# Kernel tuning notes

Measured on AMD Instinct MI355X. Metric: run time of the kernel, lower is better.

The kernel has to match this reference:

```python
import jax, jax.numpy as jnp
import numpy as np

N_NODES = 50000
N_EDGES = 600000
N_GRAPHS = 512
HID = 128
N_CLASSES = 10
N_LAYERS = 4
BN_EPS = 1e-5


def setup_inputs() -> dict:
    key = jax.random.key(0)
    ks = jax.random.split(key, 12)
    s = 1.0 / np.sqrt(HID)
    x = jax.random.normal(ks[0], (N_NODES, HID), dtype=jnp.float32)
    edge_index = jax.random.randint(ks[1], (2, N_EDGES), 0, N_NODES, dtype=jnp.int64)
    batch = jnp.sort(jax.random.randint(ks[2], (N_NODES,), 0, N_GRAPHS, dtype=jnp.int64))
    return {
        "x": x,
        "edge_index": edge_index,
        "batch": batch,
        # stacked SAGEConv params: lin_l (neighbor, with bias) and lin_r (root, no bias)
        "Wl": jax.random.uniform(ks[3], (N_LAYERS, HID, HID), jnp.float32, -s, s),
        "bl": jax.random.uniform(ks[4], (N_LAYERS, HID), jnp.float32, -s, s),
        "Wr": jax.random.uniform(ks[5], (N_LAYERS, HID, HID), jnp.float32, -s, s),
        # BatchNorm affine params per layer
        "gamma": jnp.ones((N_LAYERS, HID), jnp.float32),
        "beta": jnp.zeros((N_LAYERS, HID), jnp.float32),
        # classifier: Linear(HID, HID//2) -> ReLU -> Linear(HID//2, C)
        "W1": jax.random.uniform(ks[6], (HID // 2, HID), jnp.float32, -s, s),
        "b1": jax.random.uniform(ks[7], (HID // 2,), jnp.float32, -s, s),
        "W2": jax.random.uniform(ks[8], (N_CLASSES, HID // 2), jnp.float32, -1.0 / np.sqrt(HID // 2), 1.0 / np.sqrt(HID // 2)),
        "b2": jax.random.uniform(ks[9], (N_CLASSES,), jnp.float32, -1.0 / np.sqrt(HID // 2), 1.0 / np.sqrt(HID // 2)),
    }


def reference(x, edge_index, batch, Wl, bl, Wr, gamma, beta, W1, b1, W2, b2):
    src, dst = edge_index[0], edge_index[1]
    n = x.shape[0]
    # in-degree for mean aggregation (clamped to avoid div by zero)
    deg = jax.ops.segment_sum(jnp.ones(src.shape[0], x.dtype), dst, num_segments=n)
    inv_deg = 1.0 / jnp.maximum(deg, 1.0)  # [N]
    for l in range(Wl.shape[0]):
        # SAGEConv: mean-aggregate neighbor features, then lin_l(agg) + lin_r(x)
        agg = jax.ops.segment_sum(x[src], dst, num_segments=n) * inv_deg[:, None]  # [N,H]
        h = agg @ Wl[l].T + bl[l] + x @ Wr[l].T  # [N,H]
        # BatchNorm1d (training-mode batch stats, biased variance)
        mu = h.mean(axis=0)
        var = h.var(axis=0)
        h = (h - mu) * jax.lax.rsqrt(var + BN_EPS) * gamma[l] + beta[l]
        x = jax.nn.relu(h)  # dropout is identity in eval/reference
    # global mean pool over graphs
    cnt = jax.ops.segment_sum(jnp.ones(n, x.dtype), batch, num_segments=N_GRAPHS)
    pooled = jax.ops.segment_sum(x, batch, num_segments=N_GRAPHS) / jnp.maximum(cnt, 1.0)[:, None]
    h = jax.nn.relu(pooled @ W1.T + b1)
    return h @ W2.T + b2  # [G, C]
```

## Files before the change

kernel.cpp:

```cpp
#include <hip/hip_runtime.h>

#define NNODES 50000
#define MPAD   50048
#define NEDGES 600000
#define NGRAPHS 512
#define HID 128
#define NLAYERS 4
#define BN_EPS 1e-5f
#define GEMMBLK 391
#define PROWS 25

typedef __bf16 bf16x8 __attribute__((ext_vector_type(8)));
typedef float  f32x4  __attribute__((ext_vector_type(4)));
typedef unsigned short u16x8 __attribute__((ext_vector_type(8)));

__device__ __forceinline__ unsigned short f2bf(float f) {
    unsigned u = __builtin_bit_cast(unsigned, f);
    unsigned r = (u + 0x7fffu + ((u >> 16) & 1u)) >> 16;
    return (unsigned short)r;
}
__device__ __forceinline__ float bf2f(unsigned short u) {
    return __builtin_bit_cast(float, (unsigned)u << 16);
}

__global__ void k_init(int* __restrict__ deg,
                       int* __restrict__ pa, int* __restrict__ pb,
                       int* __restrict__ pc, int* __restrict__ pd,
                       int* __restrict__ pooled, int* __restrict__ gcnt) {
    int t = blockIdx.x * 256 + threadIdx.x;
    if (t < 50000) { deg[t] = 0; }
    int u = t - 50000;
    if (u >= 0 && u < 3072) { pa[u] = 0; pb[u] = 0; pc[u] = 0; pd[u] = 0; }
    int v = t - 53072;
    if (v >= 0 && v < 65536) pooled[v] = 0;
    int w = t - 118608;
    if (w >= 0 && w < 512) gcnt[w] = 0;
}

__global__ void k_count_deg(const int* __restrict__ dst, int* __restrict__ deg, int E) {
    int e = blockIdx.x * blockDim.x + threadIdx.x;
    if (e < E) atomicAdd(&deg[dst[e]], 1);
}

__global__ void k_scan1(const int* __restrict__ deg, int* __restrict__ exg,
                        int* __restrict__ bsum, int n) {
    __shared__ int s[512];
    int tid = threadIdx.x;
    int i = blockIdx.x * 512 + tid;
    int v = (i < n) ? deg[i] : 0;
    s[tid] = v;
    __syncthreads();
    for (int off = 1; off < 512; off <<= 1) {
        int t = (tid >= off) ? s[tid - off] : 0;
        __syncthreads();
        s[tid] += t;
        __syncthreads();
    }
    if (i < n) exg[i] = s[tid] - v;
    if (tid == 511) bsum[blockIdx.x] = s[511];
}

__global__ void k_scan2(int* __restrict__ bsum, int nb) {
    __shared__ int s[128];
    int tid = threadIdx.x;
    int v = (tid < nb) ? bsum[tid] : 0;
    s[tid] = v;
    __syncthreads();
    for (int off = 1; off < 128; off <<= 1) {
        int t = (tid >= off) ? s[tid - off] : 0;
        __syncthreads();
        s[tid] += t;
        __syncthreads();
    }
    if (tid < nb) bsum[tid] = s[tid] - v;
}

__global__ void k_scan3(const int* __restrict__ exg, const int* __restrict__ bsum,
                        const int* __restrict__ deg,
                        int* __restrict__ rowptr, int* __restrict__ cursor,
                        float* __restrict__ inv_deg, int n, int E) {
    int i = blockIdx.x * blockDim.x + threadIdx.x;
    if (i < n) {
        int r = exg[i] + bsum[i >> 9];
        rowptr[i] = r;
        cursor[i] = r;
        int d = deg[i];
        inv_deg[i] = 1.0f / (float)max(d, 1);
        if (i == 0) rowptr[n] = E;
    }
}

__global__ void k_fill_csr(const int* __restrict__ src, const int* __restrict__ dst,
                           int* __restrict__ cursor, int* __restrict__ csr_src, int E) {
    int e = blockIdx.x * blockDim.x + threadIdx.x;
    if (e < E) {
        int pos = atomicAdd(&cursor[dst[e]], 1);
        csr_src[pos] = src[e];
    }
}

__global__ void k_split(const float* __restrict__ x,
                        unsigned short* __restrict__ xhi, unsigned short* __restrict__ xlo) {
    int idx = blockIdx.x * 256 + threadIdx.x;
    float4 v = ((const float4*)x)[idx];
    ushort4 h, l;
    h.x = f2bf(v.x); l.x = f2bf(v.x - bf2f(h.x));
    h.y = f2bf(v.y); l.y = f2bf(v.y - bf2f(h.y));
    h.z = f2bf(v.z); l.z = f2bf(v.z - bf2f(h.z));
    h.w = f2bf(v.w); l.w = f2bf(v.w - bf2f(h.w));
    *(ushort4*)(xhi + (size_t)idx * 4) = h;
    *(ushort4*)(xlo + (size_t)idx * 4) = l;
}

__global__ void k_wpack(const float* __restrict__ Wl, const float* __restrict__ Wr,
                        unsigned short* __restrict__ Wpk) {
    int lane = threadIdx.x;
    int b = blockIdx.x;
    int nf = b & 7, ks = (b >> 3) & 7, l = b >> 6;
    int n = nf * 16 + (lane & 15);
    int k = ks * 32 + (lane >> 4) * 8;
    const float* W = (k < 128) ? (Wl + (size_t)l * HID * HID)
                               : (Wr + (size_t)l * HID * HID - 128);
    size_t base = ((((size_t)l * 64 + ks * 8 + nf) * 2) * 64 + lane) * 8;
    #pragma unroll
    for (int j = 0; j < 8; ++j) {
        float w = W[(size_t)n * 128 + k + j];
        unsigned short h = f2bf(w);
        unsigned short lo = f2bf(w - bf2f(h));
        Wpk[base + j] = h;
        Wpk[base + 512 + j] = lo;
    }
}

__global__ void k_aggregate5(const unsigned short* __restrict__ xhi,
                             const int* __restrict__ csr_src, const int* __restrict__ rowptr,
                             const float* __restrict__ inv_deg,
                             unsigned short* __restrict__ ahi, unsigned short* __restrict__ alo) {
    int lane = threadIdx.x & 63;
    int wid = threadIdx.x >> 6;
    int node = blockIdx.x * 4 + wid;
    int beg = rowptr[node];
    int deg = rowptr[node + 1] - beg;
    int eg = lane >> 4;
    int fo = (lane & 15) * 8;

    int idx_l = (lane < deg) ? csr_src[beg + lane] : 0;

    float acc0[8] = {0.f, 0.f, 0.f, 0.f, 0.f, 0.f, 0.f, 0.f};
    float acc1[8] = {0.f, 0.f, 0.f, 0.f, 0.f, 0.f, 0.f, 0.f};
    int dmax = min(deg, 64);
    for (int base = 0; base < dmax; base += 8) {
        int s0 = __shfl(idx_l, base + eg);
        int s1 = __shfl(idx_l, base + 4 + eg);
        if (base + eg < deg) {
            u16x8 v = *(const u16x8*)(xhi + (size_t)s0 * 128 + fo);
            #pragma unroll
            for (int j = 0; j < 8; ++j) acc0[j] += bf2f(v[j]);
        }
        if (base + 4 + eg < deg) {
            u16x8 v = *(const u16x8*)(xhi + (size_t)s1 * 128 + fo);
            #pragma unroll
            for (int j = 0; j < 8; ++j) acc1[j] += bf2f(v[j]);
        }
    }
    for (int e = beg + 64 + eg; e < beg + deg; e += 4) {
        int s = csr_src[e];
        u16x8 v = *(const u16x8*)(xhi + (size_t)s * 128 + fo);
        #pragma unroll
        for (int j = 0; j < 8; ++j) acc0[j] += bf2f(v[j]);
    }

    #pragma unroll
    for (int j = 0; j < 8; ++j) {
        float a = acc0[j] + acc1[j];
        a += __shfl_xor(a, 16);
        a += __shfl_xor(a, 32);
        acc0[j] = a;
    }
    if (lane < 16) {
        float idg = inv_deg[node];
        u16x8 hv, lv;
        #pragma unroll
        for (int j = 0; j < 8; ++j) {
            float a = acc0[j] * idg;
            unsigned short h = f2bf(a);
            hv[j] = h;
            lv[j] = f2bf(a - bf2f(h));
        }
        *(u16x8*)(ahi + (size_t)node * 128 + fo) = hv;
        *(u16x8*)(alo + (size_t)node * 128 + fo) = lv;
    }
}

__launch_bounds__(256) __global__
void k_mfma_gemm(const unsigned short* __restrict__ Ahi0, const unsigned short* __restrict__ Alo0,
                 const unsigned short* __restrict__ Ahi1, const unsigned short* __restrict__ Alo1,
                 const unsigned short* __restrict__ Wpk, const float* __restrict__ bl,
                 float* __restrict__ Hout,
                 float* __restrict__ psum, float* __restrict__ pqsum) {
    int wid = threadIdx.x >> 6;
    int lane = threadIdx.x & 63;
    int m0 = blockIdx.x * 128 + wid * 32;
    int r = lane & 15;
    int kg = lane >> 4;

    f32x4 acc[2][8];
    #pragma unroll
    for (int nf = 0; nf < 8; ++nf) {
        float b = bl[nf * 16 + r];
        acc[0][nf] = f32x4{b, b, b, b};
        acc[1][nf] = f32x4{b, b, b, b};
    }

    #pragma unroll
    for (int ks = 0; ks < 8; ++ks) {
        const unsigned short* hi = (ks < 4) ? Ahi0 : Ahi1;
        const unsigned short* lo = (ks < 4) ? Alo0 : Alo1;
        int kc = (ks & 3) * 32 + kg * 8;
        bf16x8 ah0 = *(const bf16x8*)(hi + (size_t)(m0 + r) * 128 + kc);
        bf16x8 al0 = *(const bf16x8*)(lo + (size_t)(m0 + r) * 128 + kc);
        bf16x8 ah1 = *(const bf16x8*)(hi + (size_t)(m0 + 16 + r) * 128 + kc);
        bf16x8 al1 = *(const bf16x8*)(lo + (size_t)(m0 + 16 + r) * 128 + kc);
        const unsigned short* wb = Wpk + (size_t)ks * 8192;
        #pragma unroll
        for (int nf = 0; nf < 8; ++nf) {
            bf16x8 bh = *(const bf16x8*)(wb + (size_t)nf * 1024 + lane * 8);
            bf16x8 bl2 = *(const bf16x8*)(wb + (size_t)nf * 1024 + 512 + lane * 8);
            acc[0][nf] = __builtin_amdgcn_mfma_f32_16x16x32_bf16(ah0, bh,  acc[0][nf], 0, 0, 0);
            acc[0][nf] = __builtin_amdgcn_mfma_f32_16x16x32_bf16(al0, bh,  acc[0][nf], 0, 0, 0);
            acc[0][nf] = __builtin_amdgcn_mfma_f32_16x16x32_bf16(ah0, bl2, acc[0][nf], 0, 0, 0);
            acc[1][nf] = __builtin_amdgcn_mfma_f32_16x16x32_bf16(ah1, bh,  acc[1][nf], 0, 0, 0);
            acc[1][nf] = __builtin_amdgcn_mfma_f32_16x16x32_bf16(al1, bh,  acc[1][nf], 0, 0, 0);
            acc[1][nf] = __builtin_amdgcn_mfma_f32_16x16x32_bf16(ah1, bl2, acc[1][nf], 0, 0, 0);
        }
    }

    #pragma unroll
    for (int mf = 0; mf < 2; ++mf)
        #pragma unroll
        for (int nf = 0; nf < 8; ++nf)
            #pragma unroll
            for (int g = 0; g < 4; ++g)
                Hout[(size_t)(m0 + mf * 16 + kg * 4 + g) * 128 + nf * 16 + r] = acc[mf][nf][g];

    __shared__ float ls[4][8][16];
    __shared__ float lq[4][8][16];
    #pragma unroll
    for (int nf = 0; nf < 8; ++nf) {
        float ss = 0.f, qq = 0.f;
        #pragma unroll
        for (int mf = 0; mf < 2; ++mf)
            #pragma unroll
            for (int g = 0; g < 4; ++g) {
                int row = m0 + mf * 16 + kg * 4 + g;
                float v = acc[mf][nf][g];
                float msk = (row < NNODES) ? 1.f : 0.f;
                ss += v * msk;
                qq += v * v * msk;
            }
        ss += __shfl_xor(ss, 16);
        ss += __shfl_xor(ss, 32);
        qq += __shfl_xor(qq, 16);
        qq += __shfl_xor(qq, 32);
        if (lane < 16) { ls[wid][nf][lane] = ss; lq[wid][nf][lane] = qq; }
    }
    __syncthreads();
    int t = threadIdx.x;
    if (t < 128) {
        int nf = t >> 4, rr = t & 15;
        float ssum = ls[0][nf][rr] + ls[1][nf][rr] + ls[2][nf][rr] + ls[3][nf][rr];
        float qsum = lq[0][nf][rr] + lq[1][nf][rr] + lq[2][nf][rr] + lq[3][nf][rr];
        psum[(size_t)t * GEMMBLK + blockIdx.x] = ssum;
        pqsum[(size_t)t * GEMMBLK + blockIdx.x] = qsum;
    }
}

__global__ void k_bnfin2(const float* __restrict__ psum, const float* __restrict__ pqsum,
                         const float* __restrict__ gamma, const float* __restrict__ beta,
                         float* __restrict__ scale, float* __restrict__ shift) {
    int c = blockIdx.x;
    int t = threadIdx.x;
    float s = 0.f, q = 0.f;
    const float* ps = psum + (size_t)c * GEMMBLK;
    const float* pq = pqsum + (size_t)c * GEMMBLK;
    for (int b = t; b < GEMMBLK; b += 64) { s += ps[b]; q += pq[b]; }
    #pragma unroll
    for (int off = 32; off; off >>= 1) {
        s += __shfl_xor(s, off);
        q += __shfl_xor(q, off);
    }
    if (t == 0) {
        float inv_n = 1.0f / (float)NNODES;
        float mu = s * inv_n;
        float var = q * inv_n - mu * mu;
        float is = rsqrtf(var + BN_EPS);
        float g = gamma[c] * is;
        scale[c] = g;
        shift[c] = beta[c] - mu * g;
    }
}

__global__ void k_bnrelu2(const float* __restrict__ h, const float* __restrict__ scale,
                          const float* __restrict__ shift,
                          unsigned short* __restrict__ xhi, unsigned short* __restrict__ xlo) {
    int idx = blockIdx.x * 256 + threadIdx.x;
    int cv = idx & 31;
    float4 sc = ((const float4*)scale)[cv];
    float4 sh = ((const float4*)shift)[cv];
    float4 v = ((const float4*)h)[idx];
    v.x = fmaxf(v.x * sc.x + sh.x, 0.f);
    v.y = fmaxf(v.y * sc.y + sh.y, 0.f);
    v.z = fmaxf(v.z * sc.z + sh.z, 0.f);
    v.w = fmaxf(v.w * sc.w + sh.w, 0.f);
    ushort4 hh, ll;
    hh.x = f2bf(v.x); ll.x = f2bf(v.x - bf2f(hh.x));
    hh.y = f2bf(v.y); ll.y = f2bf(v.y - bf2f(hh.y));
    hh.z = f2bf(v.z); ll.z = f2bf(v.z - bf2f(hh.z));
    hh.w = f2bf(v.w); ll.w = f2bf(v.w - bf2f(hh.w));
    *(ushort4*)(xhi + (size_t)idx * 4) = hh;
    *(ushort4*)(xlo + (size_t)idx * 4) = ll;
}

__global__ void k_pool_seg(const unsigned short* __restrict__ xhi,
                           const unsigned short* __restrict__ xlo,
                           const int* __restrict__ batch,
                           float* __restrict__ pooled, int* __restrict__ gcnt) {
    int t = threadIdx.x;
    int r0 = blockIdx.x * PROWS;
    float a0 = 0.f, a1 = 0.f;
    int cur = batch[r0];
    int seg = r0;
    for (int i = 0; i < PROWS; ++i) {
        int r = r0 + i;
        int g = batch[r];
        if (g != cur) {
            atomicAdd(&pooled[cur * 128 + 2 * t], a0);
            atomicAdd(&pooled[cur * 128 + 2 * t + 1], a1);
            if (t == 0) atomicAdd(&gcnt[cur], r - seg);
            a0 = a1 = 0.f; cur = g; seg = r;
        }
        unsigned uh = *(const unsigned*)(xhi + (size_t)r * 128 + 2 * t);
        unsigned ul = *(const unsigned*)(xlo + (size_t)r * 128 + 2 * t);
        a0 += bf2f((unsigned short)(uh & 0xffff)) + bf2f((unsigned short)(ul & 0xffff));
        a1 += bf2f((unsigned short)(uh >> 16)) + bf2f((unsigned short)(ul >> 16));
    }
    atomicAdd(&pooled[cur * 128 + 2 * t], a0);
    atomicAdd(&pooled[cur * 128 + 2 * t + 1], a1);
    if (t == 0) atomicAdd(&gcnt[cur], r0 + PROWS - seg);
}

__global__ void k_cls(const float* __restrict__ pooled, const int* __restrict__ gcnt,
                      const float* __restrict__ W1, const float* __restrict__ b1,
                      const float* __restrict__ W2, const float* __restrict__ b2,
                      float* __restrict__ out) {
    int g = blockIdx.x;
    int t = threadIdx.x;
    __shared__ float P[128];
    __shared__ float H1[64];
    float inv = 1.0f / (float)max(gcnt[g], 1);
    P[t] = pooled[g * 128 + t] * inv;
    P[t + 64] = pooled[g * 128 + 64 + t] * inv;
    __syncthreads();
    float a = b1[t];
    #pragma unroll 8
    for (int k = 0; k < 128; ++k) a += P[k] * W1[t * 128 + k];
    H1[t] = fmaxf(a, 0.f);
    __syncthreads();
    if (t < 10) {
        float a2 = b2[t];
        #pragma unroll 8
        for (int k = 0; k < 64; ++k) a2 += H1[k] * W2[t * 64 + k];
        out[g * 10 + t] = a2;
    }
}

extern "C" void kernel_launch(void* const* d_in, const int* in_sizes, int n_in,
                              void* d_out, int out_size, void* d_ws, size_t ws_size,
                              hipStream_t stream) {
    const float* x_in  = (const float*)d_in[0];
    const int*   ei    = (const int*)d_in[1];
    const int*   batch = (const int*)d_in[2];
    const float* Wl    = (const float*)d_in[3];
    const float* bl    = (const float*)d_in[4];
    const float* Wr    = (const float*)d_in[5];
    const float* gamma = (const float*)d_in[6];
    const float* beta  = (const float*)d_in[7];
    const float* W1    = (const float*)d_in[8];
    const float* b1    = (const float*)d_in[9];
    const float* W2    = (const float*)d_in[10];
    const float* b2    = (const float*)d_in[11];
    float* out = (float*)d_out;

    const int N = NNODES, E = NEDGES;
    const int* src = ei;
    const int* dst = ei + E;

    char* p = (char*)d_ws;
    auto alloc = [&](size_t bytes) {
        char* r = p;
        p += (bytes + 255) & ~(size_t)255;
        return r;
    };
    unsigned short* ahi = (unsigned short*)alloc((size_t)MPAD * HID * 2);
    unsigned short* alo = (unsigned short*)alloc((size_t)MPAD * HID * 2);
    unsigned short* xhi = (unsigned short*)alloc((size_t)MPAD * HID * 2);
    unsigned short* xlo = (unsigned short*)alloc((size_t)MPAD * HID * 2);
    float*  h        = (float*)alloc((size_t)MPAD * HID * 4);
    unsigned short* wpk = (unsigned short*)alloc((size_t)NLAYERS * 64 * 2 * 64 * 8 * 2);
    int*    deg      = (int*)alloc((size_t)N * 4);
    float*  inv_deg  = (float*)alloc((size_t)N * 4);
    int*    rowptr   = (int*)alloc((size_t)(N + 1) * 4);
    int*    cursor   = (int*)alloc((size_t)N * 4);
    int*    csr_src  = (int*)alloc((size_t)E * 4);
    int*    exg      = (int*)alloc((size_t)N * 4);
    int*    bsum     = (int*)alloc(512);
    float*  psum     = (float*)alloc((size_t)HID * GEMMBLK * 4);
    float*  pqsum    = (float*)alloc((size_t)HID * GEMMBLK * 4);
    float*  scale    = (float*)alloc(HID * 4);
    float*  shift    = (float*)alloc(HID * 4);
    float*  pooled   = (float*)alloc((size_t)NGRAPHS * HID * 4);
    int*    gcnt     = (int*)alloc((size_t)NGRAPHS * 4);

    k_init<<<502, 256, 0, stream>>>(deg,
                                    (int*)(ahi + (size_t)N * HID), (int*)(alo + (size_t)N * HID),
                                    (int*)(xhi + (size_t)N * HID), (int*)(xlo + (size_t)N * HID),
                                    (int*)pooled, gcnt);

    int eb = (E + 255) / 256;
    k_count_deg<<<eb, 256, 0, stream>>>(dst, deg, E);
    int nb = (N + 511) / 512;
    k_scan1<<<nb, 512, 0, stream>>>(deg, exg, bsum, N);
    k_scan2<<<1, 128, 0, stream>>>(bsum, nb);
    k_scan3<<<(N + 255) / 256, 256, 0, stream>>>(exg, bsum, deg, rowptr, cursor, inv_deg, N, E);
    k_fill_csr<<<eb, 256, 0, stream>>>(src, dst, cursor, csr_src, E);

    k_wpack<<<NLAYERS * 64, 64, 0, stream>>>(Wl, Wr, wpk);
    k_split<<<(N * HID / 4) / 256, 256, 0, stream>>>(x_in, xhi, xlo);

    for (int l = 0; l < NLAYERS; ++l) {
        k_aggregate5<<<N / 4, 256, 0, stream>>>(xhi, csr_src, rowptr, inv_deg, ahi, alo);
        k_mfma_gemm<<<GEMMBLK, 256, 0, stream>>>(ahi, alo, xhi, xlo,
                                                 wpk + (size_t)l * 65536,
                                                 bl + (size_t)l * HID, h, psum, pqsum);
        k_bnfin2<<<HID, 64, 0, stream>>>(psum, pqsum, gamma + (size_t)l * HID,
                                         beta + (size_t)l * HID, scale, shift);
        k_bnrelu2<<<(N * HID / 4) / 256, 256, 0, stream>>>(h, scale, shift, xhi, xlo);
    }

    k_pool_seg<<<N / PROWS, 64, 0, stream>>>(xhi, xlo, batch, pooled, gcnt);
    k_cls<<<NGRAPHS, 64, 0, stream>>>(pooled, gcnt, W1, b1, W2, b2, out);
}
```

Measured before the change: 379.4 us.

## Fuse GEMM, BatchNorm statistics and BN-ReLU into one kernel with grid barrier

Merges the MFMA GEMM, the BatchNorm finalize and the BN+ReLU+bf16 split into a single per-layer kernel. The three steps are joined by a software grid-wide atomic barrier, so the fp32 `h` intermediate never goes to global memory. This removes a full write and read-back of the hidden activations and two kernel launches per layer. In exchange, every block redundantly reduces the per-block partial sums. The final bf16 stores are narrower 2-byte scattered writes, and correctness relies on all 391 blocks being co-resident for the spin barrier.

```diff
diff --git a/kernel.cpp b/kernel.cpp
--- a/kernel.cpp
+++ b/kernel.cpp
@@ -26,7 +26,8 @@
 __global__ void k_init(int* __restrict__ deg,
                        int* __restrict__ pa, int* __restrict__ pb,
                        int* __restrict__ pc, int* __restrict__ pd,
-                       int* __restrict__ pooled, int* __restrict__ gcnt) {
+                       int* __restrict__ pooled, int* __restrict__ gcnt,
+                       unsigned* __restrict__ bar) {
     int t = blockIdx.x * 256 + threadIdx.x;
     if (t < 50000) { deg[t] = 0; }
     int u = t - 50000;
@@ -35,6 +36,8 @@
     if (v >= 0 && v < 65536) pooled[v] = 0;
     int w = t - 118608;
     if (w >= 0 && w < 512) gcnt[w] = 0;
+    int b = t - 119120;
+    if (b >= 0 && b < NLAYERS) bar[b] = 0u;
 }
 
 __global__ void k_count_deg(const int* __restrict__ dst, int* __restrict__ deg, int E) {
@@ -192,12 +195,13 @@
     }
 }
 
-__launch_bounds__(256) __global__
-void k_mfma_gemm(const unsigned short* __restrict__ Ahi0, const unsigned short* __restrict__ Alo0,
-                 const unsigned short* __restrict__ Ahi1, const unsigned short* __restrict__ Alo1,
-                 const unsigned short* __restrict__ Wpk, const float* __restrict__ bl,
-                 float* __restrict__ Hout,
-                 float* __restrict__ psum, float* __restrict__ pqsum) {
+__launch_bounds__(256, 2) __global__
+void k_layer(const unsigned short* __restrict__ Ahi, const unsigned short* __restrict__ Alo,
+             unsigned short* __restrict__ Xhi, unsigned short* __restrict__ Xlo,
+             const unsigned short* __restrict__ Wpk, const float* __restrict__ bl,
+             const float* __restrict__ gamma, const float* __restrict__ beta,
+             float* __restrict__ psum, float* __restrict__ pqsum,
+             unsigned* __restrict__ bar) {
     int wid = threadIdx.x >> 6;
     int lane = threadIdx.x & 63;
     int m0 = blockIdx.x * 128 + wid * 32;
@@ -214,8 +218,8 @@
 
     #pragma unroll
     for (int ks = 0; ks < 8; ++ks) {
-        const unsigned short* hi = (ks < 4) ? Ahi0 : Ahi1;
-        const unsigned short* lo = (ks < 4) ? Alo0 : Alo1;
+        const unsigned short* hi = (ks < 4) ? Ahi : Xhi;
+        const unsigned short* lo = (ks < 4) ? Alo : Xlo;
         int kc = (ks & 3) * 32 + kg * 8;
         bf16x8 ah0 = *(const bf16x8*)(hi + (size_t)(m0 + r) * 128 + kc);
         bf16x8 al0 = *(const bf16x8*)(lo + (size_t)(m0 + r) * 128 + kc);
@@ -234,14 +238,6 @@
             acc[1][nf] = __builtin_amdgcn_mfma_f32_16x16x32_bf16(ah1, bl2, acc[1][nf], 0, 0, 0);
         }
     }
-
-    #pragma unroll
-    for (int mf = 0; mf < 2; ++mf)
-        #pragma unroll
-        for (int nf = 0; nf < 8; ++nf)
-            #pragma unroll
-            for (int g = 0; g < 4; ++g)
-                Hout[(size_t)(m0 + mf * 16 + kg * 4 + g) * 128 + nf * 16 + r] = acc[mf][nf][g];
 
     __shared__ float ls[4][8][16];
     __shared__ float lq[4][8][16];
@@ -270,55 +266,61 @@
         int nf = t >> 4, rr = t & 15;
         float ssum = ls[0][nf][rr] + ls[1][nf][rr] + ls[2][nf][rr] + ls[3][nf][rr];
         float qsum = lq[0][nf][rr] + lq[1][nf][rr] + lq[2][nf][rr] + lq[3][nf][rr];
-        psum[(size_t)t * GEMMBLK + blockIdx.x] = ssum;
-        pqsum[(size_t)t * GEMMBLK + blockIdx.x] = qsum;
-    }
-}
-
-__global__ void k_bnfin2(const float* __restrict__ psum, const float* __restrict__ pqsum,
-                         const float* __restrict__ gamma, const float* __restrict__ beta,
-                         float* __restrict__ scale, float* __restrict__ shift) {
-    int c = blockIdx.x;
-    int t = threadIdx.x;
-    float s = 0.f, q = 0.f;
-    const float* ps = psum + (size_t)c * GEMMBLK;
-    const float* pq = pqsum + (size_t)c * GEMMBLK;
-    for (int b = t; b < GEMMBLK; b += 64) { s += ps[b]; q += pq[b]; }
-    #pragma unroll
-    for (int off = 32; off; off >>= 1) {
-        s += __shfl_xor(s, off);
-        q += __shfl_xor(q, off);
-    }
+        psum[(size_t)blockIdx.x * 128 + t] = ssum;
+        pqsum[(size_t)blockIdx.x * 128 + t] = qsum;
+    }
+
+    __threadfence();
+    __syncthreads();
     if (t == 0) {
+        __hip_atomic_fetch_add(bar, 1u, __ATOMIC_ACQ_REL, __HIP_MEMORY_SCOPE_AGENT);
+        while (__hip_atomic_load(bar, __ATOMIC_ACQUIRE, __HIP_MEMORY_SCOPE_AGENT) < (unsigned)GEMMBLK)
+            __builtin_amdgcn_s_sleep(2);
+    }
+    __syncthreads();
+    __threadfence();
+
+    __shared__ float sS[256], sQ[256];
+    __shared__ float scaleS[128], shiftS[128];
+    {
+        float s = 0.f, q = 0.f;
+        int c = t & 127;
+        for (int b = (t >> 7); b < GEMMBLK; b += 2) {
+            s += psum[(size_t)b * 128 + c];
+            q += pqsum[(size_t)b * 128 + c];
+        }
+        sS[t] = s; sQ[t] = q;
+    }
+    __syncthreads();
+    if (t < 128) {
+        float ss = sS[t] + sS[t + 128];
+        float qq = sQ[t] + sQ[t + 128];
         float inv_n = 1.0f / (float)NNODES;
-        float mu = s * inv_n;
-        float var = q * inv_n - mu * mu;
+        float mu = ss * inv_n;
+        float var = qq * inv_n - mu * mu;
         float is = rsqrtf(var + BN_EPS);
-        float g = gamma[c] * is;
-        scale[c] = g;
-        shift[c] = beta[c] - mu * g;
-    }
-}
-
-__global__ void k_bnrelu2(const float* __restrict__ h, const float* __restrict__ scale,
-                          const float* __restrict__ shift,
-                          unsigned short* __restrict__ xhi, unsigned short* __restrict__ xlo) {
-    int idx = blockIdx.x * 256 + threadIdx.x;
-    int cv = idx & 31;
-    float4 sc = ((const float4*)scale)[cv];
-    float4 sh = ((const float4*)shift)[cv];
-    float4 v = ((const float4*)h)[idx];
-    v.x = fmaxf(v.x * sc.x + sh.x, 0.f);
-    v.y = fmaxf(v.y * sc.y + sh.y, 0.f);
-    v.z = fmaxf(v.z * sc.z + sh.z, 0.f);
-    v.w = fmaxf(v.w * sc.w + sh.w, 0.f);
-    ushort4 hh, ll;
-    hh.x = f2bf(v.x); ll.x = f2bf(v.x - bf2f(hh.x));
-    hh.y = f2bf(v.y); ll.y = f2bf(v.y - bf2f(hh.y));
-    hh.z = f2bf(v.z); ll.z = f2bf(v.z - bf2f(hh.z));
-    hh.w = f2bf(v.w); ll.w = f2bf(v.w - bf2f(hh.w));
-    *(ushort4*)(xhi + (size_t)idx * 4) = hh;
-    *(ushort4*)(xlo + (size_t)idx * 4) = ll;
+        float g = gamma[t] * is;
+        scaleS[t] = g;
+        shiftS[t] = beta[t] - mu * g;
+    }
+    __syncthreads();
+
+    #pragma unroll
+    for (int mf = 0; mf < 2; ++mf)
+        #pragma unroll
+        for (int nf = 0; nf < 8; ++nf) {
+            int col = nf * 16 + r;
+            float sc = scaleS[col];
+            float sh = shiftS[col];
+            #pragma unroll
+            for (int g = 0; g < 4; ++g) {
+                int row = m0 + mf * 16 + kg * 4 + g;
+                float v = fmaxf(acc[mf][nf][g] * sc + sh, 0.f);
+                unsigned short hh = f2bf(v);
+                Xhi[(size_t)row * 128 + col] = hh;
+                Xlo[(size_t)row * 128 + col] = f2bf(v - bf2f(hh));
+            }
+        }
 }
 
 __global__ void k_pool_seg(const unsigned short* __restrict__ xhi,
@@ -405,7 +407,6 @@
     unsigned short* alo = (unsigned short*)alloc((size_t)MPAD * HID * 2);
     unsigned short* xhi = (unsigned short*)alloc((size_t)MPAD * HID * 2);
     unsigned short* xlo = (unsigned short*)alloc((size_t)MPAD * HID * 2);
-    float*  h        = (float*)alloc((size_t)MPAD * HID * 4);
     unsigned short* wpk = (unsigned short*)alloc((size_t)NLAYERS * 64 * 2 * 64 * 8 * 2);
     int*    deg      = (int*)alloc((size_t)N * 4);
     float*  inv_deg  = (float*)alloc((size_t)N * 4);
@@ -416,15 +417,14 @@
     int*    bsum     = (int*)alloc(512);
     float*  psum     = (float*)alloc((size_t)HID * GEMMBLK * 4);
     float*  pqsum    = (float*)alloc((size_t)HID * GEMMBLK * 4);
-    float*  scale    = (float*)alloc(HID * 4);
-    float*  shift    = (float*)alloc(HID * 4);
     float*  pooled   = (float*)alloc((size_t)NGRAPHS * HID * 4);
     int*    gcnt     = (int*)alloc((size_t)NGRAPHS * 4);
+    unsigned* bar    = (unsigned*)alloc(NLAYERS * 4);
 
     k_init<<<502, 256, 0, stream>>>(deg,
                                     (int*)(ahi + (size_t)N * HID), (int*)(alo + (size_t)N * HID),
                                     (int*)(xhi + (size_t)N * HID), (int*)(xlo + (size_t)N * HID),
-                                    (int*)pooled, gcnt);
+                                    (int*)pooled, gcnt, bar);
 
     int eb = (E + 255) / 256;
     k_count_deg<<<eb, 256, 0, stream>>>(dst, deg, E);
@@ -439,12 +439,11 @@
 
     for (int l = 0; l < NLAYERS; ++l) {
         k_aggregate5<<<N / 4, 256, 0, stream>>>(xhi, csr_src, rowptr, inv_deg, ahi, alo);
-        k_mfma_gemm<<<GEMMBLK, 256, 0, stream>>>(ahi, alo, xhi, xlo,
-                                                 wpk + (size_t)l * 65536,
-                                                 bl + (size_t)l * HID, h, psum, pqsum);
-        k_bnfin2<<<HID, 64, 0, stream>>>(psum, pqsum, gamma + (size_t)l * HID,
-                                         beta + (size_t)l * HID, scale, shift);
-        k_bnrelu2<<<(N * HID / 4) / 256, 256, 0, stream>>>(h, scale, shift, xhi, xlo);
+        k_layer<<<GEMMBLK, 256, 0, stream>>>(ahi, alo, xhi, xlo,
+                                             wpk + (size_t)l * 65536,
+                                             bl + (size_t)l * HID,
+                                             gamma + (size_t)l * HID, beta + (size_t)l * HID,
+                                             psum, pqsum, bar + l);
     }
 
     k_pool_seg<<<N / PROWS, 64, 0, stream>>>(xhi, xlo, batch, pooled, gcnt);
```

Measured after the change: 882.4 us. 2.33x slower.

## Store node features in 32-column blocks and aggregate one feature block per pass

Applied to the files above, without the earlier changes.

Node feature and aggregate buffers (hi/lo bf16 splits) change from row-major 128-wide rows to four feature blocks of 32 columns each. The neighbor-mean aggregation then runs four passes, one per block, so each gather touches a smaller working set that has a better chance of staying in L2. The split, BN/ReLU, GEMM, pooling and padding-zeroing kernels are all rewritten to use the new indexing. The trade-off is 64-byte gathers instead of 256-byte ones, four times as many aggregation blocks, and CSR indices that are re-read on every pass.

```diff
diff --git a/kernel.cpp b/kernel.cpp
--- a/kernel.cpp
+++ b/kernel.cpp
@@ -9,6 +9,7 @@
 #define BN_EPS 1e-5f
 #define GEMMBLK 391
 #define PROWS 25
+#define FBLK  (MPAD * 32)
 
 typedef __bf16 bf16x8 __attribute__((ext_vector_type(8)));
 typedef float  f32x4  __attribute__((ext_vector_type(4)));
@@ -22,6 +23,7 @@
 __device__ __forceinline__ float bf2f(unsigned short u) {
     return __builtin_bit_cast(float, (unsigned)u << 16);
 }
+
 
 __global__ void k_init(int* __restrict__ deg,
                        int* __restrict__ pa, int* __restrict__ pb,
@@ -30,7 +32,11 @@
     int t = blockIdx.x * 256 + threadIdx.x;
     if (t < 50000) { deg[t] = 0; }
     int u = t - 50000;
-    if (u >= 0 && u < 3072) { pa[u] = 0; pb[u] = 0; pc[u] = 0; pd[u] = 0; }
+    if (u >= 0 && u < 3072) {
+        int blk = u / 768, off = u - blk * 768;
+        int idx = blk * (MPAD * 16) + 50000 * 16 + off;
+        pa[idx] = 0; pb[idx] = 0; pc[idx] = 0; pd[idx] = 0;
+    }
     int v = t - 53072;
     if (v >= 0 && v < 65536) pooled[v] = 0;
     int w = t - 118608;
@@ -102,14 +108,16 @@
 __global__ void k_split(const float* __restrict__ x,
                         unsigned short* __restrict__ xhi, unsigned short* __restrict__ xlo) {
     int idx = blockIdx.x * 256 + threadIdx.x;
+    int row = idx >> 5, q = idx & 31;
     float4 v = ((const float4*)x)[idx];
     ushort4 h, l;
     h.x = f2bf(v.x); l.x = f2bf(v.x - bf2f(h.x));
     h.y = f2bf(v.y); l.y = f2bf(v.y - bf2f(h.y));
     h.z = f2bf(v.z); l.z = f2bf(v.z - bf2f(h.z));
     h.w = f2bf(v.w); l.w = f2bf(v.w - bf2f(h.w));
-    *(ushort4*)(xhi + (size_t)idx * 4) = h;
-    *(ushort4*)(xlo + (size_t)idx * 4) = l;
+    size_t dst = (size_t)(q >> 3) * FBLK + (size_t)row * 32 + (q & 7) * 4;
+    *(ushort4*)(xhi + dst) = h;
+    *(ushort4*)(xlo + dst) = l;
 }
 
 __global__ void k_wpack(const float* __restrict__ Wl, const float* __restrict__ Wr,
@@ -132,69 +140,65 @@
     }
 }
 
-__global__ void k_aggregate5(const unsigned short* __restrict__ xhi,
+__global__ void k_aggregate6(const unsigned short* __restrict__ xhi,
                              const int* __restrict__ csr_src, const int* __restrict__ rowptr,
                              const float* __restrict__ inv_deg,
                              unsigned short* __restrict__ ahi, unsigned short* __restrict__ alo) {
     int lane = threadIdx.x & 63;
     int wid = threadIdx.x >> 6;
-    int node = blockIdx.x * 4 + wid;
+    int nb   = blockIdx.x % 12500;
+    int pass = blockIdx.x / 12500;
+    int node = nb * 4 + wid;
     int beg = rowptr[node];
     int deg = rowptr[node + 1] - beg;
-    int eg = lane >> 4;
-    int fo = (lane & 15) * 8;
+    int slot = lane >> 2;
+    int f    = lane & 3;
+    size_t bb = (size_t)pass * FBLK;
 
     int idx_l = (lane < deg) ? csr_src[beg + lane] : 0;
 
-    float acc0[8] = {0.f, 0.f, 0.f, 0.f, 0.f, 0.f, 0.f, 0.f};
-    float acc1[8] = {0.f, 0.f, 0.f, 0.f, 0.f, 0.f, 0.f, 0.f};
+    float acc[8] = {0.f, 0.f, 0.f, 0.f, 0.f, 0.f, 0.f, 0.f};
     int dmax = min(deg, 64);
-    for (int base = 0; base < dmax; base += 8) {
-        int s0 = __shfl(idx_l, base + eg);
-        int s1 = __shfl(idx_l, base + 4 + eg);
-        if (base + eg < deg) {
-            u16x8 v = *(const u16x8*)(xhi + (size_t)s0 * 128 + fo);
+    for (int base = 0; base < dmax; base += 16) {
+        int s0 = __shfl(idx_l, base + slot);
+        if (base + slot < deg) {
+            u16x8 v = *(const u16x8*)(xhi + bb + (size_t)s0 * 32 + f * 8);
             #pragma unroll
-            for (int j = 0; j < 8; ++j) acc0[j] += bf2f(v[j]);
+            for (int j = 0; j < 8; ++j) acc[j] += bf2f(v[j]);
         }
-        if (base + 4 + eg < deg) {
-            u16x8 v = *(const u16x8*)(xhi + (size_t)s1 * 128 + fo);
-            #pragma unroll
-            for (int j = 0; j < 8; ++j) acc1[j] += bf2f(v[j]);
-        }
-    }
-    for (int e = beg + 64 + eg; e < beg + deg; e += 4) {
+    }
+    for (int e = beg + 64 + slot; e < beg + deg; e += 16) {
         int s = csr_src[e];
-        u16x8 v = *(const u16x8*)(xhi + (size_t)s * 128 + fo);
+        u16x8 v = *(const u16x8*)(xhi + bb + (size_t)s * 32 + f * 8);
         #pragma unroll
-        for (int j = 0; j < 8; ++j) acc0[j] += bf2f(v[j]);
+        for (int j = 0; j < 8; ++j) acc[j] += bf2f(v[j]);
     }
 
     #pragma unroll
     for (int j = 0; j < 8; ++j) {
-        float a = acc0[j] + acc1[j];
-        a += __shfl_xor(a, 16);
-        a += __shfl_xor(a, 32);
-        acc0[j] = a;
-    }
-    if (lane < 16) {
+        acc[j] += __shfl_xor(acc[j], 4);
+        acc[j] += __shfl_xor(acc[j], 8);
+        acc[j] += __shfl_xor(acc[j], 16);
+        acc[j] += __shfl_xor(acc[j], 32);
+    }
+    if (lane < 4) {
         float idg = inv_deg[node];
         u16x8 hv, lv;
         #pragma unroll
         for (int j = 0; j < 8; ++j) {
-            float a = acc0[j] * idg;
+            float a = acc[j] * idg;
             unsigned short h = f2bf(a);
             hv[j] = h;
             lv[j] = f2bf(a - bf2f(h));
         }
-        *(u16x8*)(ahi + (size_t)node * 128 + fo) = hv;
-        *(u16x8*)(alo + (size_t)node * 128 + fo) = lv;
+        *(u16x8*)(ahi + bb + (size_t)node * 32 + f * 8) = hv;
+        *(u16x8*)(alo + bb + (size_t)node * 32 + f * 8) = lv;
     }
 }
 
 __launch_bounds__(256) __global__
-void k_mfma_gemm(const unsigned short* __restrict__ Ahi0, const unsigned short* __restrict__ Alo0,
-                 const unsigned short* __restrict__ Ahi1, const unsigned short* __restrict__ Alo1,
+void k_mfma_gemm(const unsigned short* __restrict__ Ahi, const unsigned short* __restrict__ Alo,
+                 const unsigned short* __restrict__ Xhi, const unsigned short* __restrict__ Xlo,
                  const unsigned short* __restrict__ Wpk, const float* __restrict__ bl,
                  float* __restrict__ Hout,
                  float* __restrict__ psum, float* __restrict__ pqsum) {
@@ -214,13 +218,13 @@
 
     #pragma unroll
     for (int ks = 0; ks < 8; ++ks) {
-        const unsigned short* hi = (ks < 4) ? Ahi0 : Ahi1;
-        const unsigned short* lo = (ks < 4) ? Alo0 : Alo1;
-        int kc = (ks & 3) * 32 + kg * 8;
-        bf16x8 ah0 = *(const bf16x8*)(hi + (size_t)(m0 + r) * 128 + kc);
-        bf16x8 al0 = *(const bf16x8*)(lo + (size_t)(m0 + r) * 128 + kc);
-        bf16x8 ah1 = *(const bf16x8*)(hi + (size_t)(m0 + 16 + r) * 128 + kc);
-        bf16x8 al1 = *(const bf16x8*)(lo + (size_t)(m0 + 16 + r) * 128 + kc);
+        const unsigned short* hi = (ks < 4) ? Ahi : Xhi;
+        const unsigned short* lo = (ks < 4) ? Alo : Xlo;
+        size_t bb = (size_t)(ks & 3) * FBLK + kg * 8;
+        bf16x8 ah0 = *(const bf16x8*)(hi + bb + (size_t)(m0 + r) * 32);
+        bf16x8 al0 = *(const bf16x8*)(lo + bb + (size_t)(m0 + r) * 32);
+        bf16x8 ah1 = *(const bf16x8*)(hi + bb + (size_t)(m0 + 16 + r) * 32);
+        bf16x8 al1 = *(const bf16x8*)(lo + bb + (size_t)(m0 + 16 + r) * 32);
         const unsigned short* wb = Wpk + (size_t)ks * 8192;
         #pragma unroll
         for (int nf = 0; nf < 8; ++nf) {
@@ -304,9 +308,9 @@
                           const float* __restrict__ shift,
                           unsigned short* __restrict__ xhi, unsigned short* __restrict__ xlo) {
     int idx = blockIdx.x * 256 + threadIdx.x;
-    int cv = idx & 31;
-    float4 sc = ((const float4*)scale)[cv];
-    float4 sh = ((const float4*)shift)[cv];
+    int row = idx >> 5, q = idx & 31;
+    float4 sc = ((const float4*)scale)[q];
+    float4 sh = ((const float4*)shift)[q];
     float4 v = ((const float4*)h)[idx];
     v.x = fmaxf(v.x * sc.x + sh.x, 0.f);
     v.y = fmaxf(v.y * sc.y + sh.y, 0.f);
@@ -317,8 +321,9 @@
     hh.y = f2bf(v.y); ll.y = f2bf(v.y - bf2f(hh.y));
     hh.z = f2bf(v.z); ll.z = f2bf(v.z - bf2f(hh.z));
     hh.w = f2bf(v.w); ll.w = f2bf(v.w - bf2f(hh.w));
-    *(ushort4*)(xhi + (size_t)idx * 4) = hh;
-    *(ushort4*)(xlo + (size_t)idx * 4) = ll;
+    size_t dst = (size_t)(q >> 3) * FBLK + (size_t)row * 32 + (q & 7) * 4;
+    *(ushort4*)(xhi + dst) = hh;
+    *(ushort4*)(xlo + dst) = ll;
 }
 
 __global__ void k_pool_seg(const unsigned short* __restrict__ xhi,
@@ -327,6 +332,7 @@
                            float* __restrict__ pooled, int* __restrict__ gcnt) {
     int t = threadIdx.x;
     int r0 = blockIdx.x * PROWS;
+    size_t bb = (size_t)(t >> 4) * FBLK + ((2 * t) & 31);
     float a0 = 0.f, a1 = 0.f;
     int cur = batch[r0];
     int seg = r0;
@@ -339,8 +345,8 @@
             if (t == 0) atomicAdd(&gcnt[cur], r - seg);
             a0 = a1 = 0.f; cur = g; seg = r;
         }
-        unsigned uh = *(const unsigned*)(xhi + (size_t)r * 128 + 2 * t);
-        unsigned ul = *(const unsigned*)(xlo + (size_t)r * 128 + 2 * t);
+        unsigned uh = *(const unsigned*)(xhi + bb + (size_t)r * 32);
+        unsigned ul = *(const unsigned*)(xlo + bb + (size_t)r * 32);
         a0 += bf2f((unsigned short)(uh & 0xffff)) + bf2f((unsigned short)(ul & 0xffff));
         a1 += bf2f((unsigned short)(uh >> 16)) + bf2f((unsigned short)(ul >> 16));
     }
@@ -421,9 +427,7 @@
     float*  pooled   = (float*)alloc((size_t)NGRAPHS * HID * 4);
     int*    gcnt     = (int*)alloc((size_t)NGRAPHS * 4);
 
-    k_init<<<502, 256, 0, stream>>>(deg,
-                                    (int*)(ahi + (size_t)N * HID), (int*)(alo + (size_t)N * HID),
-                                    (int*)(xhi + (size_t)N * HID), (int*)(xlo + (size_t)N * HID),
+    k_init<<<466, 256, 0, stream>>>(deg, (int*)ahi, (int*)alo, (int*)xhi, (int*)xlo,
                                     (int*)pooled, gcnt);
 
     int eb = (E + 255) / 256;
@@ -438,7 +442,7 @@
     k_split<<<(N * HID / 4) / 256, 256, 0, stream>>>(x_in, xhi, xlo);
 
     for (int l = 0; l < NLAYERS; ++l) {
-        k_aggregate5<<<N / 4, 256, 0, stream>>>(xhi, csr_src, rowptr, inv_deg, ahi, alo);
+        k_aggregate6<<<4 * 12500, 256, 0, stream>>>(xhi, csr_src, rowptr, inv_deg, ahi, alo);
         k_mfma_gemm<<<GEMMBLK, 256, 0, stream>>>(ahi, alo, xhi, xlo,
                                                  wpk + (size_t)l * 65536,
                                                  bl + (size_t)l * HID, h, psum, pqsum);
```

Measured after the change: 551.3 us, median of 2. 45.3% more time.
